# Kernel tuning notes

Hardware: AMD Instinct MI355X
Metric: run time of the kernel (lower is better)

Reference implementation:

```python
import jax, jax.numpy as jnp
import numpy as np

B, S, D, H = 8, 2048, 1024, 64

def setup_inputs() -> dict:
    key = jax.random.key(0)
    ks = jax.random.split(key, 7)
    scale = 0.02
    return {
        "x": jax.random.normal(ks[0], (B, S, D), dtype=jnp.float32),
        "Wq": jax.random.normal(ks[1], (D, H), dtype=jnp.float32) * scale,
        "bq": jax.random.normal(ks[2], (H,), dtype=jnp.float32) * scale,
        "Wk": jax.random.normal(ks[3], (D, H), dtype=jnp.float32) * scale,
        "bk": jax.random.normal(ks[4], (H,), dtype=jnp.float32) * scale,
        "Wv": jax.random.normal(ks[5], (D, H), dtype=jnp.float32) * scale,
        "bv": jax.random.normal(ks[6], (H,), dtype=jnp.float32) * scale,
    }

def reference(x, Wq, bq, Wk, bk, Wv, bv):
    # Single-head causal self-attention (dropout in eval mode -> identity).
    q = x @ Wq + bq            # [B,S,H]
    k = x @ Wk + bk            # [B,S,H]
    v = x @ Wv + bv            # [B,S,H]
    scores = jnp.einsum("bqh,bkh->bqk", q, k)  # [B,S,S]
    s = q.shape[1]
    causal = jnp.tril(jnp.ones((s, s), dtype=bool))
    # Original masks with -inf BEFORE scaling; -inf/scale == -inf, so equivalent.
    scores = jnp.where(causal, scores, -jnp.inf) / jnp.sqrt(jnp.float32(k.shape[-1]))
    attn = jax.nn.softmax(scores, axis=-1)
    return jnp.einsum("bqk,bkh->bqh", attn, v)
```

## Files before the change

### kernel.cpp

```cpp
#include <hip/hip_runtime.h>
#include <math.h>

#define BATCH 8
#define SEQ   2048
#define DIM   1024
#define HD    64
#define NROWS (BATCH * SEQ)
#define CHUNK 256
#define NCHUNK 8
#define QTILE 64
#define NQT   (SEQ / QTILE)
#define QSCALE 0.1803368801f

typedef __attribute__((ext_vector_type(8))) short bf16x8;
typedef __attribute__((ext_vector_type(4))) float f32x4;

__device__ __forceinline__ unsigned short f2bf(float f) {
    unsigned u = __float_as_uint(f);
    u = (u + 0x7FFFu + ((u >> 16) & 1u)) >> 16;
    return (unsigned short)u;
}
__device__ __forceinline__ unsigned short f2bf_hu(float f) {
    return (unsigned short)((__float_as_uint(f) + 0x8000u) >> 16);
}
__device__ __forceinline__ float fast_exp2(float x) {
#if __has_builtin(__builtin_amdgcn_exp2f)
    return __builtin_amdgcn_exp2f(x);
#else
    return exp2f(x);
#endif
}

__device__ __forceinline__ void gld_lds16(const void* g, void* l) {
    __builtin_amdgcn_global_load_lds(
        (const __attribute__((address_space(1))) void*)g,
        (__attribute__((address_space(3))) void*)l, 16, 0, 0);
}

__device__ __forceinline__ uint4 pack_bf16x8(float4 a, float4 b) {
    uint4 o;
    o.x = ((__float_as_uint(a.x) + 0x8000u) >> 16) | ((__float_as_uint(a.y) + 0x8000u) & 0xFFFF0000u);
    o.y = ((__float_as_uint(a.z) + 0x8000u) >> 16) | ((__float_as_uint(a.w) + 0x8000u) & 0xFFFF0000u);
    o.z = ((__float_as_uint(b.x) + 0x8000u) >> 16) | ((__float_as_uint(b.y) + 0x8000u) & 0xFFFF0000u);
    o.w = ((__float_as_uint(b.z) + 0x8000u) >> 16) | ((__float_as_uint(b.w) + 0x8000u) & 0xFFFF0000u);
    return o;
}


__global__ __launch_bounds__(256)
void prep_w_kernel(const float* __restrict__ Wq, const float* __restrict__ Wk,
                   const float* __restrict__ Wv, unsigned short* __restrict__ Wt)
{
    const int mat = blockIdx.y;
    const float* __restrict__ W = (mat == 0) ? Wq : (mat == 1) ? Wk : Wv;
    const int k0 = blockIdx.x * 64;
    __shared__ float T[64][65];
    const int t = threadIdx.x;
    #pragma unroll
    for (int i = 0; i < 16; ++i) {
        const int idx = t + i * 256;
        T[idx >> 6][idx & 63] = W[(size_t)(k0 + (idx >> 6)) * HD + (idx & 63)];
    }
    __syncthreads();
    const int n = t >> 2;
    const int c = t & 3;
    union { unsigned short h[16]; uint4 v[2]; } buf;
    #pragma unroll
    for (int j = 0; j < 16; ++j) buf.h[j] = f2bf(T[c * 16 + j][n]);
    unsigned short* dst = Wt + ((size_t)mat * HD + n) * DIM + k0 + c * 16;
    *(uint4*)dst       = buf.v[0];
    *(uint4*)(dst + 8) = buf.v[1];
}

__global__ __launch_bounds__(384)
void qkv_mfma_kernel(const float* __restrict__ x,
                     const unsigned short* __restrict__ Wt,
                     const float* __restrict__ bq, const float* __restrict__ bk,
                     const float* __restrict__ bv,
                     unsigned short* __restrict__ Qg,
                     unsigned short* __restrict__ Kg,
                     unsigned short* __restrict__ Vtg)
{
    __shared__ unsigned short Xs[2][32][64];
    __shared__ unsigned short Ws[2][192][64];

    const int t    = threadIdx.x;
    const int lane = t & 63;
    const int w    = t >> 6;
    const int col  = lane & 15;
    const int quad = lane >> 4;
    const int rh   = w & 1;
    const int mat  = w >> 1;
    const int row0 = blockIdx.x * 32;

    const int r8  = lane >> 3;
    const int ch8 = lane & 7;
    const int wswz = (ch8 ^ r8) * 8;

    f32x4 acc[4];
    #pragma unroll
    for (int i = 0; i < 4; ++i) acc[i] = (f32x4){0.f, 0.f, 0.f, 0.f};

    const int xr  = t >> 3;
    const int xc0 = t & 7;
    const float* __restrict__ xrow = &x[(size_t)(row0 + xr) * DIM];

    #pragma unroll
    for (int ii = 0; ii < 4; ++ii) {
        const int rbase = w * 32 + ii * 8;
        gld_lds16(&Wt[(size_t)(rbase + r8) * DIM + wswz], &Ws[0][rbase][0]);
    }
    float4 xa, xb;
    if (t < 256) {
        xa = *(const float4*)(xrow + xc0 * 8);
        xb = *(const float4*)(xrow + xc0 * 8 + 4);
        *(uint4*)&Xs[0][xr][(xc0 ^ (xr & 7)) * 8] = pack_bf16x8(xa, xb);
    }
    __syncthreads();

    int buf = 0;
    for (int it = 0; it < 16; ++it) {
        if (it < 15) {
            const int k0n = (it + 1) * 64;
            #pragma unroll
            for (int ii = 0; ii < 4; ++ii) {
                const int rbase = w * 32 + ii * 8;
                gld_lds16(&Wt[(size_t)(rbase + r8) * DIM + k0n + wswz],
                          &Ws[buf ^ 1][rbase][0]);
            }
            if (t < 256) {
                xa = *(const float4*)(xrow + k0n + xc0 * 8);
                xb = *(const float4*)(xrow + k0n + xc0 * 8 + 4);
            }
        }
        #pragma unroll
        for (int ks = 0; ks < 2; ++ks) {
            const int fswz = ((ks * 4 + quad) ^ (col & 7)) * 8;
            const bf16x8 a = *(const bf16x8*)&Xs[buf][rh * 16 + col][fswz];
            #pragma unroll
            for (int nt = 0; nt < 4; ++nt) {
                const bf16x8 b = *(const bf16x8*)&Ws[buf][mat * 64 + nt * 16 + col][fswz];
                acc[nt] = __builtin_amdgcn_mfma_f32_16x16x32_bf16(a, b, acc[nt], 0, 0, 0);
            }
        }
        __syncthreads();
        if (it < 15 && t < 256)
            *(uint4*)&Xs[buf ^ 1][xr][(xc0 ^ (xr & 7)) * 8] = pack_bf16x8(xa, xb);
        __syncthreads();
        buf ^= 1;
    }

    const int b    = row0 / SEQ;
    const int s0   = (row0 % SEQ) + rh * 16 + quad * 4;
    const int grow = row0 + rh * 16 + quad * 4;
    const float* __restrict__ bias = (mat == 0) ? bq : (mat == 1) ? bk : bv;
    const float oscale = (mat == 0) ? QSCALE : 1.0f;
    #pragma unroll
    for (int nt = 0; nt < 4; ++nt) {
        const int nn = nt * 16 + col;
        const float bvv = bias[nn];
        if (mat < 2) {
            unsigned short* __restrict__ o = (mat == 0) ? Qg : Kg;
            #pragma unroll
            for (int r = 0; r < 4; ++r)
                o[(size_t)(grow + r) * HD + nn] = f2bf((acc[nt][r] + bvv) * oscale);
        } else {
            const unsigned lo = (unsigned)f2bf(acc[nt][0] + bvv) | ((unsigned)f2bf(acc[nt][1] + bvv) << 16);
            const unsigned hi = (unsigned)f2bf(acc[nt][2] + bvv) | ((unsigned)f2bf(acc[nt][3] + bvv) << 16);
            *(uint2*)&Vtg[((size_t)b * HD + nn) * SEQ + s0] = make_uint2(lo, hi);
        }
    }
}

__global__ __launch_bounds__(256)
void attn_part_kernel(const unsigned short* __restrict__ Qg,
                      const unsigned short* __restrict__ Kg,
                      const unsigned short* __restrict__ Vtg,
                      unsigned short* __restrict__ Opart,
                      float* __restrict__ Lsum)
{
    const int b = blockIdx.x;
    int y = blockIdx.y, c = 0;
    while (y >= 32 - 4 * c) { y -= 32 - 4 * c; ++c; }
    const int qt = y + 4 * c;

    __shared__ unsigned short Ks[64][64];
    __shared__ unsigned short Vs[64][64];
    __shared__ unsigned short Ps[4][16][76];

    const int t    = threadIdx.x;
    const int w    = t >> 6;
    const int lane = t & 63;
    const int col  = lane & 15;
    const int quad = lane >> 4;
    const int q0w  = qt * QTILE + w * 16;
    const size_t gq = (size_t)b * SEQ + q0w;

    const bf16x8 aq0 = *(const bf16x8*)&Qg[(gq + col) * HD + quad * 8];
    const bf16x8 aq1 = *(const bf16x8*)&Qg[(gq + col) * HD + 32 + quad * 8];

    f32x4 oacc[4];
    #pragma unroll
    for (int n = 0; n < 4; ++n) oacc[n] = (f32x4){0.f, 0.f, 0.f, 0.f};
    float lpart[4] = {0.f, 0.f, 0.f, 0.f};

    const int kbeg   = c * CHUNK;
    const int kend   = min((c + 1) * CHUNK, (qt + 1) * QTILE);
    const int ntiles = (kend - kbeg + 63) >> 6;

    const int r8 = lane >> 3, ch = lane & 7;
    const int swzr = (ch ^ r8) * 8;
    const unsigned short* kgb = Kg  + (size_t)b * SEQ * HD;
    const unsigned short* vgb = Vtg + (size_t)b * HD * SEQ;

    for (int it = 0; it < ntiles; ++it) {
        const int j0 = kbeg + it * 64;
        __syncthreads();
        #pragma unroll
        for (int ii = 0; ii < 2; ++ii) {
            const int rb = w * 16 + ii * 8;
            gld_lds16(&kgb[(size_t)(j0 + rb + r8) * HD + swzr], &Ks[rb][0]);
            gld_lds16(&vgb[(size_t)(rb + r8) * SEQ + j0 + swzr], &Vs[rb][0]);
        }
        __syncthreads();

        if (j0 <= q0w + 15) {
            f32x4 scv[4];
            #pragma unroll
            for (int nt = 0; nt < 4; ++nt) {
                const int sw0 = (quad ^ (col & 7)) * 8;
                const int sw1 = ((4 + quad) ^ (col & 7)) * 8;
                const bf16x8 bk0 = *(const bf16x8*)&Ks[nt * 16 + col][sw0];
                const bf16x8 bk1 = *(const bf16x8*)&Ks[nt * 16 + col][sw1];
                f32x4 s = __builtin_amdgcn_mfma_f32_16x16x32_bf16(aq0, bk0, (f32x4){0.f,0.f,0.f,0.f}, 0, 0, 0);
                s = __builtin_amdgcn_mfma_f32_16x16x32_bf16(aq1, bk1, s, 0, 0, 0);
                scv[nt] = s;
            }
            const bool needmask = (j0 + 63 > q0w);
            #pragma unroll
            for (int r = 0; r < 4; ++r) {
                const int row = q0w + quad * 4 + r;
                #pragma unroll
                for (int nt = 0; nt < 4; ++nt) {
                    float s = scv[nt][r];
                    if (needmask)
                        s = (j0 + nt * 16 + col <= row) ? s : -INFINITY;
                    const float p = fast_exp2(s);
                    lpart[r] += p;
                    Ps[w][quad * 4 + r][nt * 16 + col] = f2bf_hu(p);
                }
            }
            #pragma unroll
            for (int ks = 0; ks < 2; ++ks) {
                const bf16x8 ap = *(const bf16x8*)&Ps[w][col][ks * 32 + quad * 8];
                const int fswz = ((ks * 4 + quad) ^ (col & 7)) * 8;
                #pragma unroll
                for (int n = 0; n < 4; ++n) {
                    const bf16x8 bv2 = *(const bf16x8*)&Vs[n * 16 + col][fswz];
                    oacc[n] = __builtin_amdgcn_mfma_f32_16x16x32_bf16(ap, bv2, oacc[n], 0, 0, 0);
                }
            }
        }
    }

    #pragma unroll
    for (int r = 0; r < 4; ++r) {
        #pragma unroll
        for (int off = 1; off < 16; off <<= 1)
            lpart[r] += __shfl_xor(lpart[r], off, 64);
    }

    const int blk = (b * NQT + qt) * NCHUNK + c;
    unsigned short* Ob = Opart + (size_t)blk * (QTILE * HD);
    #pragma unroll
    for (int n = 0; n < 4; ++n)
        #pragma unroll
        for (int r = 0; r < 4; ++r)
            Ob[(w * 16 + quad * 4 + r) * HD + n * 16 + col] = f2bf(oacc[n][r]);
    if (col == 0) {
        float* lb = Lsum + (size_t)blk * QTILE;
        #pragma unroll
        for (int r = 0; r < 4; ++r)
            lb[w * 16 + quad * 4 + r] = lpart[r];
    }
}

__global__ __launch_bounds__(256)
void combine_kernel(const unsigned short* __restrict__ Opart,
                    const float* __restrict__ Lsum,
                    float* __restrict__ out)
{
    const int gid = blockIdx.x * 256 + threadIdx.x;
    const int i   = gid >> 4;
    const int d4  = (gid & 15) * 4;
    const int b   = i >> 11;
    const int s   = i & 2047;
    const int qt  = s >> 6;
    const int r64 = s & 63;
    const int nc  = (s >> 8) + 1;
    const int blk0 = (b * NQT + qt) * NCHUNK;

    float L = 0.f;
    float a0 = 0.f, a1 = 0.f, a2 = 0.f, a3 = 0.f;
    for (int cc = 0; cc < nc; ++cc) {
        L += Lsum[(size_t)(blk0 + cc) * QTILE + r64];
        const uint2 u = *(const uint2*)(Opart + (size_t)(blk0 + cc) * (QTILE * HD) + r64 * HD + d4);
        a0 += __uint_as_float(u.x << 16);
        a1 += __uint_as_float(u.x & 0xFFFF0000u);
        a2 += __uint_as_float(u.y << 16);
        a3 += __uint_as_float(u.y & 0xFFFF0000u);
    }
    const float rL = 1.0f / L;
    float4 o; o.x = a0 * rL; o.y = a1 * rL; o.z = a2 * rL; o.w = a3 * rL;
    *(float4*)&out[(size_t)i * HD + d4] = o;
}

extern "C" void kernel_launch(void* const* d_in, const int* in_sizes, int n_in,
                              void* d_out, int out_size, void* d_ws, size_t ws_size,
                              hipStream_t stream) {
    const float* x  = (const float*)d_in[0];
    const float* Wq = (const float*)d_in[1];
    const float* bq = (const float*)d_in[2];
    const float* Wk = (const float*)d_in[3];
    const float* bk = (const float*)d_in[4];
    const float* Wv = (const float*)d_in[5];
    const float* bv = (const float*)d_in[6];
    float* out = (float*)d_out;

    unsigned short* Wt    = (unsigned short*)d_ws;
    unsigned short* Qg    = Wt + (size_t)3 * HD * DIM;
    unsigned short* Kg    = Qg + (size_t)NROWS * HD;
    unsigned short* Vtg   = Kg + (size_t)NROWS * HD;
    unsigned short* Opart = Vtg + (size_t)BATCH * HD * SEQ;
    float* Lsum = (float*)(Opart + (size_t)BATCH * NQT * NCHUNK * QTILE * HD);

    prep_w_kernel<<<dim3(16, 3), 256, 0, stream>>>(Wq, Wk, Wv, Wt);
    qkv_mfma_kernel<<<dim3(NROWS / 32), 384, 0, stream>>>(x, Wt, bq, bk, bv, Qg, Kg, Vtg);
    attn_part_kernel<<<dim3(8, 144), 256, 0, stream>>>(Qg, Kg, Vtg, Opart, Lsum);
    combine_kernel<<<dim3(NROWS * 16 / 256), 256, 0, stream>>>(Opart, Lsum, out);
}
```

Before: 151.4 us.

## Stage x tile via direct global-to-LDS loads and convert to bf16 at fragment read

The QKV projection kernel now loads the fp32 x tile straight into LDS with global_load_lds, using a swizzled layout, instead of routing it through registers and packing to bf16 before the store. The bf16 conversion moves into the compute step, where each fragment is read from LDS. The two __syncthreads per iteration become raw barriers paired with explicit vmcnt waits, so the next tile's loads stay in flight during the current MFMAs. In exchange the X buffer doubles in LDS size, the conversion is repeated on every fragment read, and correctness depends on hand-counted vmcnt values.

New measurement: 151.3 us. About the same (-0.1%).

```diff
diff --git a/kernel.cpp b/kernel.cpp
--- a/kernel.cpp
+++ b/kernel.cpp
@@ -46,6 +46,8 @@
     return o;
 }
 
+#define CFENCE() asm volatile("" ::: "memory")
+#define RAW_BAR() do { CFENCE(); __builtin_amdgcn_s_barrier(); CFENCE(); } while (0)
 
 __global__ __launch_bounds__(256)
 void prep_w_kernel(const float* __restrict__ Wq, const float* __restrict__ Wk,
@@ -81,7 +83,7 @@
                      unsigned short* __restrict__ Kg,
                      unsigned short* __restrict__ Vtg)
 {
-    __shared__ unsigned short Xs[2][32][64];
+    __shared__ float          Xs[2][32][64];
     __shared__ unsigned short Ws[2][192][64];
 
     const int t    = threadIdx.x;
@@ -97,56 +99,68 @@
     const int ch8 = lane & 7;
     const int wswz = (ch8 ^ r8) * 8;
 
+    const int xr4 = lane >> 4;
+    const int xch = lane & 15;
+
     f32x4 acc[4];
     #pragma unroll
     for (int i = 0; i < 4; ++i) acc[i] = (f32x4){0.f, 0.f, 0.f, 0.f};
 
-    const int xr  = t >> 3;
-    const int xc0 = t & 7;
-    const float* __restrict__ xrow = &x[(size_t)(row0 + xr) * DIM];
-
-    #pragma unroll
-    for (int ii = 0; ii < 4; ++ii) {
-        const int rbase = w * 32 + ii * 8;
-        gld_lds16(&Wt[(size_t)(rbase + r8) * DIM + wswz], &Ws[0][rbase][0]);
-    }
-    float4 xa, xb;
-    if (t < 256) {
-        xa = *(const float4*)(xrow + xc0 * 8);
-        xb = *(const float4*)(xrow + xc0 * 8 + 4);
-        *(uint4*)&Xs[0][xr][(xc0 ^ (xr & 7)) * 8] = pack_bf16x8(xa, xb);
-    }
-    __syncthreads();
+    auto stageW = [&](int it, int bb) {
+        const int k0 = it * 64;
+        #pragma unroll
+        for (int ii = 0; ii < 4; ++ii) {
+            const int rbase = w * 32 + ii * 8;
+            gld_lds16(&Wt[(size_t)(rbase + r8) * DIM + k0 + wswz], &Ws[bb][rbase][0]);
+        }
+    };
+    auto stageX = [&](int it, int bb) {
+        const int k0 = it * 64;
+        #pragma unroll
+        for (int ii = 0; ii < 2; ++ii) {
+            const int rl = w * 8 + ii * 4;
+            const int rr = rl + xr4;
+            gld_lds16(&x[(size_t)(row0 + rr) * DIM + k0 + ((xch ^ (rr & 15)) << 2)],
+                      &Xs[bb][rl][0]);
+        }
+    };
+    auto compute = [&](int bb) {
+        #pragma unroll
+        for (int ks = 0; ks < 2; ++ks) {
+            const int c0 = ks * 8 + quad * 2;
+            const float* xsr = &Xs[bb][rh * 16 + col][0];
+            const float4 u0 = *(const float4*)(xsr + ((c0 ^ col) << 2));
+            const float4 u1 = *(const float4*)(xsr + (((c0 + 1) ^ col) << 2));
+            union { uint4 u; bf16x8 h; } av;
+            av.u = pack_bf16x8(u0, u1);
+            const int fswz = ((ks * 4 + quad) ^ (col & 7)) * 8;
+            #pragma unroll
+            for (int nt = 0; nt < 4; ++nt) {
+                const bf16x8 b = *(const bf16x8*)&Ws[bb][mat * 64 + nt * 16 + col][fswz];
+                acc[nt] = __builtin_amdgcn_mfma_f32_16x16x32_bf16(av.h, b, acc[nt], 0, 0, 0);
+            }
+        }
+    };
+
+    stageW(0, 0);
+    if (w < 4) stageX(0, 0);
 
     int buf = 0;
     for (int it = 0; it < 16; ++it) {
+        RAW_BAR();
         if (it < 15) {
-            const int k0n = (it + 1) * 64;
-            #pragma unroll
-            for (int ii = 0; ii < 4; ++ii) {
-                const int rbase = w * 32 + ii * 8;
-                gld_lds16(&Wt[(size_t)(rbase + r8) * DIM + k0n + wswz],
-                          &Ws[buf ^ 1][rbase][0]);
-            }
-            if (t < 256) {
-                xa = *(const float4*)(xrow + k0n + xc0 * 8);
-                xb = *(const float4*)(xrow + k0n + xc0 * 8 + 4);
-            }
-        }
-        #pragma unroll
-        for (int ks = 0; ks < 2; ++ks) {
-            const int fswz = ((ks * 4 + quad) ^ (col & 7)) * 8;
-            const bf16x8 a = *(const bf16x8*)&Xs[buf][rh * 16 + col][fswz];
-            #pragma unroll
-            for (int nt = 0; nt < 4; ++nt) {
-                const bf16x8 b = *(const bf16x8*)&Ws[buf][mat * 64 + nt * 16 + col][fswz];
-                acc[nt] = __builtin_amdgcn_mfma_f32_16x16x32_bf16(a, b, acc[nt], 0, 0, 0);
-            }
-        }
-        __syncthreads();
-        if (it < 15 && t < 256)
-            *(uint4*)&Xs[buf ^ 1][xr][(xc0 ^ (xr & 7)) * 8] = pack_bf16x8(xa, xb);
-        __syncthreads();
+            stageW(it + 1, buf ^ 1);
+            if (w < 4) {
+                stageX(it + 1, buf ^ 1);
+                asm volatile("s_waitcnt vmcnt(6)" ::: "memory");
+            } else {
+                asm volatile("s_waitcnt vmcnt(4)" ::: "memory");
+            }
+        } else {
+            asm volatile("s_waitcnt vmcnt(0)" ::: "memory");
+        }
+        RAW_BAR();
+        compute(buf);
         buf ^= 1;
     }
 
```

## Double QKV projection row tile and deepen x prefetch with raw barriers

Applied to the files above, without the earlier changes.

The QKV projection block now covers 64 rows with 768 threads (12 waves), so each staged weight tile is reused across twice as many rows. The x prefetch is pushed two iterations ahead, and the two __syncthreads per iteration are replaced by raw s_barrier plus explicit vmcnt waits. This is meant to cut weight traffic from L2 and hide global load latency. In exchange the block needs more registers and LDS, there are fewer blocks to fill the CUs, and correctness now depends on hand-counted vmcnt values.

Result: faster. 138.9 us (-8.3%).

```diff
diff --git a/kernel.cpp b/kernel.cpp
--- a/kernel.cpp
+++ b/kernel.cpp
@@ -46,6 +46,8 @@
     return o;
 }
 
+#define CFENCE() asm volatile("" ::: "memory")
+#define RAW_BAR() do { CFENCE(); __builtin_amdgcn_s_barrier(); CFENCE(); } while (0)
 
 __global__ __launch_bounds__(256)
 void prep_w_kernel(const float* __restrict__ Wq, const float* __restrict__ Wk,
@@ -72,7 +74,7 @@
     *(uint4*)(dst + 8) = buf.v[1];
 }
 
-__global__ __launch_bounds__(384)
+__global__ __launch_bounds__(768)
 void qkv_mfma_kernel(const float* __restrict__ x,
                      const unsigned short* __restrict__ Wt,
                      const float* __restrict__ bq, const float* __restrict__ bk,
@@ -81,7 +83,7 @@
                      unsigned short* __restrict__ Kg,
                      unsigned short* __restrict__ Vtg)
 {
-    __shared__ unsigned short Xs[2][32][64];
+    __shared__ unsigned short Xs[2][64][64];
     __shared__ unsigned short Ws[2][192][64];
 
     const int t    = threadIdx.x;
@@ -89,9 +91,9 @@
     const int w    = t >> 6;
     const int col  = lane & 15;
     const int quad = lane >> 4;
-    const int rh   = w & 1;
-    const int mat  = w >> 1;
-    const int row0 = blockIdx.x * 32;
+    const int mat  = w >> 2;
+    const int wr   = w & 3;
+    const int row0 = blockIdx.x * 64;
 
     const int r8  = lane >> 3;
     const int ch8 = lane & 7;
@@ -105,54 +107,65 @@
     const int xc0 = t & 7;
     const float* __restrict__ xrow = &x[(size_t)(row0 + xr) * DIM];
 
-    #pragma unroll
-    for (int ii = 0; ii < 4; ++ii) {
-        const int rbase = w * 32 + ii * 8;
-        gld_lds16(&Wt[(size_t)(rbase + r8) * DIM + wswz], &Ws[0][rbase][0]);
-    }
+    auto stageW = [&](int it, int bb) {
+        const int k0 = it * 64;
+        #pragma unroll
+        for (int ii = 0; ii < 2; ++ii) {
+            const int rbase = w * 16 + ii * 8;
+            gld_lds16(&Wt[(size_t)(rbase + r8) * DIM + k0 + wswz], &Ws[bb][rbase][0]);
+        }
+    };
+    auto computeT = [&](int bb) {
+        #pragma unroll
+        for (int ks = 0; ks < 2; ++ks) {
+            const int fswz = ((ks * 4 + quad) ^ (col & 7)) * 8;
+            const bf16x8 a = *(const bf16x8*)&Xs[bb][wr * 16 + col][fswz];
+            #pragma unroll
+            for (int nt = 0; nt < 4; ++nt) {
+                const bf16x8 b = *(const bf16x8*)&Ws[bb][mat * 64 + nt * 16 + col][fswz];
+                acc[nt] = __builtin_amdgcn_mfma_f32_16x16x32_bf16(a, b, acc[nt], 0, 0, 0);
+            }
+        }
+    };
+
     float4 xa, xb;
-    if (t < 256) {
+    stageW(0, 0);
+    if (t < 512) {
         xa = *(const float4*)(xrow + xc0 * 8);
         xb = *(const float4*)(xrow + xc0 * 8 + 4);
+    }
+    asm volatile("s_waitcnt vmcnt(0)" ::: "memory");
+    if (t < 512) {
         *(uint4*)&Xs[0][xr][(xc0 ^ (xr & 7)) * 8] = pack_bf16x8(xa, xb);
-    }
-    __syncthreads();
+        xa = *(const float4*)(xrow + 64 + xc0 * 8);
+        xb = *(const float4*)(xrow + 64 + xc0 * 8 + 4);
+    }
 
     int buf = 0;
     for (int it = 0; it < 16; ++it) {
+        RAW_BAR();
         if (it < 15) {
-            const int k0n = (it + 1) * 64;
-            #pragma unroll
-            for (int ii = 0; ii < 4; ++ii) {
-                const int rbase = w * 32 + ii * 8;
-                gld_lds16(&Wt[(size_t)(rbase + r8) * DIM + k0n + wswz],
-                          &Ws[buf ^ 1][rbase][0]);
-            }
-            if (t < 256) {
-                xa = *(const float4*)(xrow + k0n + xc0 * 8);
-                xb = *(const float4*)(xrow + k0n + xc0 * 8 + 4);
-            }
-        }
-        #pragma unroll
-        for (int ks = 0; ks < 2; ++ks) {
-            const int fswz = ((ks * 4 + quad) ^ (col & 7)) * 8;
-            const bf16x8 a = *(const bf16x8*)&Xs[buf][rh * 16 + col][fswz];
-            #pragma unroll
-            for (int nt = 0; nt < 4; ++nt) {
-                const bf16x8 b = *(const bf16x8*)&Ws[buf][mat * 64 + nt * 16 + col][fswz];
-                acc[nt] = __builtin_amdgcn_mfma_f32_16x16x32_bf16(a, b, acc[nt], 0, 0, 0);
-            }
-        }
-        __syncthreads();
-        if (it < 15 && t < 256)
-            *(uint4*)&Xs[buf ^ 1][xr][(xc0 ^ (xr & 7)) * 8] = pack_bf16x8(xa, xb);
-        __syncthreads();
+            stageW(it + 1, buf ^ 1);
+            asm volatile("s_waitcnt vmcnt(2)" ::: "memory");
+            if (t < 512) {
+                *(uint4*)&Xs[buf ^ 1][xr][(xc0 ^ (xr & 7)) * 8] = pack_bf16x8(xa, xb);
+                if (it < 14) {
+                    const float* xp = xrow + (it + 2) * 64;
+                    xa = *(const float4*)(xp + xc0 * 8);
+                    xb = *(const float4*)(xp + xc0 * 8 + 4);
+                }
+            }
+        } else {
+            asm volatile("s_waitcnt vmcnt(0)" ::: "memory");
+        }
+        RAW_BAR();
+        computeT(buf);
         buf ^= 1;
     }
 
     const int b    = row0 / SEQ;
-    const int s0   = (row0 % SEQ) + rh * 16 + quad * 4;
-    const int grow = row0 + rh * 16 + quad * 4;
+    const int s0   = (row0 % SEQ) + wr * 16 + quad * 4;
+    const int grow = row0 + wr * 16 + quad * 4;
     const float* __restrict__ bias = (mat == 0) ? bq : (mat == 1) ? bk : bv;
     const float oscale = (mat == 0) ? QSCALE : 1.0f;
     #pragma unroll
@@ -335,7 +348,7 @@
     float* Lsum = (float*)(Opart + (size_t)BATCH * NQT * NCHUNK * QTILE * HD);
 
     prep_w_kernel<<<dim3(16, 3), 256, 0, stream>>>(Wq, Wk, Wv, Wt);
-    qkv_mfma_kernel<<<dim3(NROWS / 32), 384, 0, stream>>>(x, Wt, bq, bk, bv, Qg, Kg, Vtg);
+    qkv_mfma_kernel<<<dim3(NROWS / 64), 768, 0, stream>>>(x, Wt, bq, bk, bv, Qg, Kg, Vtg);
     attn_part_kernel<<<dim3(8, 144), 256, 0, stream>>>(Qg, Kg, Vtg, Opart, Lsum);
     combine_kernel<<<dim3(NROWS * 16 / 256), 256, 0, stream>>>(Opart, Lsum, out);
 }
```
